# Performance work log

Hardware: AMD Instinct MI355X
Metric: run time of the kernel (lower is better)

## Reference

```python
import jax, jax.numpy as jnp
import numpy as np

B, S, D, H, R, N, RK = 2, 2048, 1024, 16, 64, 32, 128
DH = D // H
EPS = 1e-5


def setup_inputs() -> dict:
    key = jax.random.key(0)
    ks = jax.random.split(key, 24)
    f = lambda i, shape, sc=1.0: jax.random.normal(ks[i], shape, dtype=jnp.float32) * sc
    sm = lambda i, shape: jax.nn.softmax(f(i, shape), axis=-1)
    return {
        'x': f(0, (B, S, D)),
        'f_qk': f(1, (N, D, R), 0.02), 'f_v': f(2, (N, D, R), 0.02),
        'r_qk': f(3, (N, R, D), 0.02), 'r_v': f(4, (N, R, D), 0.02),
        'f_know': f(5, (N, D, RK), 0.02), 'r_know': f(6, (N, RK, D), 0.02),
        'W_O': f(7, (D, D), 0.02),
        'gamma1': jnp.ones(D, jnp.float32), 'beta1': jnp.zeros(D, jnp.float32),
        'gamma2': jnp.ones(D, jnp.float32), 'beta2': jnp.zeros(D, jnp.float32),
        'w_fq': sm(8, (B, S, N)), 'w_fk': sm(9, (B, S, N)), 'w_fv': sm(10, (B, S, N)),
        'w_rq': sm(11, (B, S, N)), 'w_rk': sm(12, (B, S, N)), 'w_rv': sm(13, (B, S, N)),
        'w_know_f': sm(14, (B, S, N)), 'w_know_r': sm(15, (B, S, N)),
    }


def _ln(x, g, b):
    mu = jnp.mean(x, axis=-1, keepdims=True)
    var = jnp.mean(jnp.square(x - mu), axis=-1, keepdims=True)
    return g * (x - mu) * jax.lax.rsqrt(var + EPS) + b


def _feature(x, neurons, w):
    # x [B,S,D], neurons [N,D,R], w [B,S,N] -> [B,S,R]
    all_h = jnp.einsum('bsd,ndr->bsnr', x, neurons)
    return jnp.einsum('bsnr,bsn->bsr', all_h, w)


def _restore(h, neurons, w):
    # h [B,S,R], neurons [N,R,D], w [B,S,N] -> [B,S,D]
    # fuse: avoid materializing [B,S,N,D]; outer-product [B,S,N,R] is small
    t = w[..., None] * h[:, :, None, :]
    return jnp.einsum('bsnr,nrd->bsd', t, neurons)


def _causal_attn(Q, K, V):
    # Q,K,V: [B,H,S,DH]
    scale = 1.0 / jnp.sqrt(jnp.asarray(DH, Q.dtype))
    scores = jnp.einsum('bhqd,bhkd->bhqk', Q, K) * scale
    mask = jnp.tril(jnp.ones((S, S), bool))
    scores = jnp.where(mask, scores, jnp.asarray(-jnp.inf, scores.dtype))
    probs = jax.nn.softmax(scores, axis=-1)
    return jnp.einsum('bhqk,bhkd->bhqd', probs, V)


def reference(x, f_qk, f_v, r_qk, r_v, f_know, r_know, W_O,
              gamma1, beta1, gamma2, beta2,
              w_fq, w_fk, w_fv, w_rq, w_rk, w_rv, w_know_f, w_know_r):
    # --- attention circuit ---
    nx = _ln(x, gamma1, beta1)
    h_q = _feature(nx, f_qk, w_fq)
    h_k = _feature(nx, f_qk, w_fk)
    h_v = _feature(nx, f_v, w_fv)
    Q = _restore(h_q, r_qk, w_rq)
    K = _restore(h_k, r_qk, w_rk)
    V = _restore(h_v, r_v, w_rv)
    to_heads = lambda t: t.reshape(B, S, H, DH).transpose(0, 2, 1, 3)
    attn = _causal_attn(to_heads(Q), to_heads(K), to_heads(V))
    attn = attn.transpose(0, 2, 1, 3).reshape(B, S, D)
    attn_out = attn @ W_O.T  # nn.Linear(d_model, d_model, bias=False)
    x = x + attn_out
    # --- knowledge circuit ---
    nx2 = _ln(x, gamma2, beta2)
    h = _feature(nx2, f_know, w_know_f)
    know_out = _restore(h, r_know, w_know_r)
    x = x + know_out
    return x
```

## Files before the change

### kernel.cpp

```cpp
#include <hip/hip_runtime.h>
#include <stdint.h>


typedef __bf16 bf16x8 __attribute__((ext_vector_type(8)));
typedef float f32x4 __attribute__((ext_vector_type(4)));

__device__ __forceinline__ unsigned short f2b(float f) {
  union { float f; unsigned u; } v; v.f = f;
  unsigned u = v.u;
  unsigned r = (u + 0x7FFFu + ((u >> 16) & 1u)) >> 16;
  return (unsigned short)r;
}
__device__ __forceinline__ float b2f(unsigned short h) {
  union { unsigned u; float f; } v; v.u = ((unsigned)h) << 16;
  return v.f;
}
__device__ __forceinline__ unsigned pk2(float lo, float hi) {
  return (unsigned)f2b(lo) | ((unsigned)f2b(hi) << 16);
}
__device__ __forceinline__ unsigned pkt(float lo, float hi) {
  union { float f; unsigned u; } a, b; a.f = lo; b.f = hi;
  return __builtin_amdgcn_perm(b.u, a.u, 0x07060302u);
}

__global__ __launch_bounds__(256, 3) void gemm_bt(
    const unsigned short* __restrict__ A, const unsigned short* __restrict__ Bt,
    void* __restrict__ out, int M, int N, int K) {
  __shared__ unsigned short lsA[128 * 64];
  __shared__ unsigned short lsB[128 * 64];
  const int tid = threadIdx.x;
  const int w = tid >> 6, lane = tid & 63;
  const int quad = lane >> 4, l16 = lane & 15;
  const int wr = w >> 1, wc = w & 1;
  const int row0 = blockIdx.y * 128;
  const int col0 = blockIdx.x * 128;

  const int srow = w * 32 + (lane >> 3);
  const int scg = ((lane & 7) ^ (lane >> 3)) * 8;
  const unsigned short* ap = A + (size_t)(row0 + srow) * K + scg;
  const unsigned short* bp = Bt + (size_t)(col0 + srow) * K + scg;

  const f32x4 fz = {0.f, 0.f, 0.f, 0.f};
  f32x4 acc[4][4];
#pragma unroll
  for (int i = 0; i < 4; ++i)
#pragma unroll
    for (int j = 0; j < 4; ++j) acc[i][j] = fz;

  for (int k0 = 0; k0 < K; k0 += 64) {
#pragma unroll
    for (int i = 0; i < 4; ++i) {
      __builtin_amdgcn_global_load_lds(
          (const __attribute__((address_space(1))) unsigned int*)(ap + (size_t)i * 8 * K + k0),
          (__attribute__((address_space(3))) unsigned int*)&lsA[(w * 32 + i * 8) * 64],
          16, 0, 0);
      __builtin_amdgcn_global_load_lds(
          (const __attribute__((address_space(1))) unsigned int*)(bp + (size_t)i * 8 * K + k0),
          (__attribute__((address_space(3))) unsigned int*)&lsB[(w * 32 + i * 8) * 64],
          16, 0, 0);
    }
    __syncthreads();
#pragma unroll
    for (int kk = 0; kk < 2; ++kk) {
      bf16x8 af[4], bfr[4];
      const int sl = (((kk * 4 + quad) ^ (l16 & 7)) * 8);
#pragma unroll
      for (int mt = 0; mt < 4; ++mt)
        af[mt] = *(const bf16x8*)&lsA[(wr * 64 + mt * 16 + l16) * 64 + sl];
#pragma unroll
      for (int nt = 0; nt < 4; ++nt)
        bfr[nt] = *(const bf16x8*)&lsB[(wc * 64 + nt * 16 + l16) * 64 + sl];
#pragma unroll
      for (int mt = 0; mt < 4; ++mt)
#pragma unroll
        for (int nt = 0; nt < 4; ++nt)
          acc[mt][nt] = __builtin_amdgcn_mfma_f32_16x16x32_bf16(af[mt], bfr[nt], acc[mt][nt], 0, 0, 0);
    }
    __syncthreads();
  }

  const int rb = row0 + wr * 64;
  const int cb = col0 + wc * 64;
#pragma unroll
  for (int mt = 0; mt < 4; ++mt) {
#pragma unroll
    for (int nt = 0; nt < 4; ++nt) {
      const int r = rb + mt * 16 + quad * 4;
      const int c = cb + nt * 16 + l16;
#pragma unroll
      for (int i = 0; i < 4; ++i)
        ((unsigned short*)out)[(size_t)(r + i) * N + c] = f2b(acc[mt][nt][i]);
    }
  }
}

__global__ __launch_bounds__(256, 3) void gemm_qkv(
    const unsigned short* __restrict__ t_qk, const unsigned short* __restrict__ t_v,
    const unsigned short* __restrict__ r_qkT, const unsigned short* __restrict__ r_vT,
    unsigned short* __restrict__ QK, unsigned short* __restrict__ VT) {
  __shared__ unsigned short lsA[128 * 64];
  __shared__ unsigned short lsB[128 * 64];
  const int K = 2048;
  const int bid = blockIdx.x;
  const unsigned short* A;
  const unsigned short* Bt;
  int row0, col0, isv;
  if (bid < 256) {
    const int xcd = bid & 7, j = bid >> 3;
    row0 = (xcd * 4 + (j >> 3)) * 128;
    col0 = (j & 7) * 128;
    A = t_v; Bt = r_vT; isv = 1;
  } else {
    const int u = bid - 256;
    const int xcd = u & 7, j = u >> 3;
    row0 = (xcd * 8 + (j >> 3)) * 128;
    col0 = (j & 7) * 128;
    A = t_qk; Bt = r_qkT; isv = 0;
  }
  const int tid = threadIdx.x;
  const int w = tid >> 6, lane = tid & 63;
  const int quad = lane >> 4, l16 = lane & 15;
  const int wr = w >> 1, wc = w & 1;

  const int srow = w * 32 + (lane >> 3);
  const int scg = ((lane & 7) ^ (lane >> 3)) * 8;
  const unsigned short* ap = A + (size_t)(row0 + srow) * K + scg;
  const unsigned short* bp = Bt + (size_t)(col0 + srow) * K + scg;

  const f32x4 fz = {0.f, 0.f, 0.f, 0.f};
  f32x4 acc[4][4];
#pragma unroll
  for (int i = 0; i < 4; ++i)
#pragma unroll
    for (int jj = 0; jj < 4; ++jj) acc[i][jj] = fz;

  for (int k0 = 0; k0 < K; k0 += 64) {
#pragma unroll
    for (int i = 0; i < 4; ++i) {
      __builtin_amdgcn_global_load_lds(
          (const __attribute__((address_space(1))) unsigned int*)(ap + (size_t)i * 8 * K + k0),
          (__attribute__((address_space(3))) unsigned int*)&lsA[(w * 32 + i * 8) * 64],
          16, 0, 0);
      __builtin_amdgcn_global_load_lds(
          (const __attribute__((address_space(1))) unsigned int*)(bp + (size_t)i * 8 * K + k0),
          (__attribute__((address_space(3))) unsigned int*)&lsB[(w * 32 + i * 8) * 64],
          16, 0, 0);
    }
    __syncthreads();
#pragma unroll
    for (int kk = 0; kk < 2; ++kk) {
      bf16x8 af[4], bfr[4];
      const int sl = (((kk * 4 + quad) ^ (l16 & 7)) * 8);
#pragma unroll
      for (int mt = 0; mt < 4; ++mt)
        af[mt] = *(const bf16x8*)&lsA[(wr * 64 + mt * 16 + l16) * 64 + sl];
#pragma unroll
      for (int nt = 0; nt < 4; ++nt)
        bfr[nt] = *(const bf16x8*)&lsB[(wc * 64 + nt * 16 + l16) * 64 + sl];
#pragma unroll
      for (int mt = 0; mt < 4; ++mt)
#pragma unroll
        for (int nt = 0; nt < 4; ++nt)
          acc[mt][nt] = __builtin_amdgcn_mfma_f32_16x16x32_bf16(af[mt], bfr[nt], acc[mt][nt], 0, 0, 0);
    }
    __syncthreads();
  }

  const int rb = row0 + wr * 64;
  const int cb = col0 + wc * 64;
#pragma unroll
  for (int mt = 0; mt < 4; ++mt) {
#pragma unroll
    for (int nt = 0; nt < 4; ++nt) {
      const int r = rb + mt * 16 + quad * 4;
      const int c = cb + nt * 16 + l16;
#pragma unroll
      for (int i = 0; i < 4; ++i) {
        const float v = acc[mt][nt][i];
        if (isv) VT[(size_t)c * 4096 + (r + i)] = f2b(v);
        else QK[(size_t)(r + i) * 1024 + c] = f2b(v);
      }
    }
  }
}

__global__ __launch_bounds__(256, 3) void gemm_ks4(
    const unsigned short* __restrict__ A, const unsigned short* __restrict__ Bt,
    float* __restrict__ p0, float* __restrict__ p1,
    float* __restrict__ p2, float* __restrict__ p3, int K) {
  __shared__ unsigned short lsA[128 * 64];
  __shared__ unsigned short lsB[128 * 64];
  const int N = 1024;
  const int bid = blockIdx.x;
  const int xcd = bid & 7, j = bid >> 3;
  const int row_l = j >> 5, rem = j & 31;
  const int ks = rem >> 3, col = rem & 7;
  const int row0 = (xcd * 4 + row_l) * 128;
  const int col0 = col * 128;
  const int kq = K >> 2;
  const int kbeg = ks * kq, kend = kbeg + kq;
  const int tid = threadIdx.x;
  const int w = tid >> 6, lane = tid & 63;
  const int quad = lane >> 4, l16 = lane & 15;
  const int wr = w >> 1, wc = w & 1;

  const int srow = w * 32 + (lane >> 3);
  const int scg = ((lane & 7) ^ (lane >> 3)) * 8;
  const unsigned short* ap = A + (size_t)(row0 + srow) * K + scg;
  const unsigned short* bp = Bt + (size_t)(col0 + srow) * K + scg;

  const f32x4 fz = {0.f, 0.f, 0.f, 0.f};
  f32x4 acc[4][4];
#pragma unroll
  for (int i = 0; i < 4; ++i)
#pragma unroll
    for (int jj = 0; jj < 4; ++jj) acc[i][jj] = fz;

  for (int k0 = kbeg; k0 < kend; k0 += 64) {
#pragma unroll
    for (int i = 0; i < 4; ++i) {
      __builtin_amdgcn_global_load_lds(
          (const __attribute__((address_space(1))) unsigned int*)(ap + (size_t)i * 8 * K + k0),
          (__attribute__((address_space(3))) unsigned int*)&lsA[(w * 32 + i * 8) * 64],
          16, 0, 0);
      __builtin_amdgcn_global_load_lds(
          (const __attribute__((address_space(1))) unsigned int*)(bp + (size_t)i * 8 * K + k0),
          (__attribute__((address_space(3))) unsigned int*)&lsB[(w * 32 + i * 8) * 64],
          16, 0, 0);
    }
    __syncthreads();
#pragma unroll
    for (int kk = 0; kk < 2; ++kk) {
      bf16x8 af[4], bfr[4];
      const int sl = (((kk * 4 + quad) ^ (l16 & 7)) * 8);
#pragma unroll
      for (int mt = 0; mt < 4; ++mt)
        af[mt] = *(const bf16x8*)&lsA[(wr * 64 + mt * 16 + l16) * 64 + sl];
#pragma unroll
      for (int nt = 0; nt < 4; ++nt)
        bfr[nt] = *(const bf16x8*)&lsB[(wc * 64 + nt * 16 + l16) * 64 + sl];
#pragma unroll
      for (int mt = 0; mt < 4; ++mt)
#pragma unroll
        for (int nt = 0; nt < 4; ++nt)
          acc[mt][nt] = __builtin_amdgcn_mfma_f32_16x16x32_bf16(af[mt], bfr[nt], acc[mt][nt], 0, 0, 0);
    }
    __syncthreads();
  }

  float* out = (ks == 0) ? p0 : (ks == 1) ? p1 : (ks == 2) ? p2 : p3;
  const int rb = row0 + wr * 64;
  const int cb = col0 + wc * 64;
#pragma unroll
  for (int mt = 0; mt < 4; ++mt) {
#pragma unroll
    for (int nt = 0; nt < 4; ++nt) {
      const int r = rb + mt * 16 + quad * 4;
      const int c = cb + nt * 16 + l16;
#pragma unroll
      for (int i = 0; i < 4; ++i)
        out[(size_t)(r + i) * N + c] = acc[mt][nt][i];
    }
  }
}

__global__ __launch_bounds__(256) void gemm_wo_res(
    const unsigned short* __restrict__ A, const unsigned short* __restrict__ Bt,
    const float* __restrict__ res, float* __restrict__ out) {
  __shared__ unsigned short lsA[128 * 64];
  __shared__ unsigned short lsB[64 * 64];
  const int K = 1024, N = 1024;
  const int bid = blockIdx.x;
  const int xcd = bid & 7, j = bid >> 3;
  const int row0 = (xcd * 4 + (j & 3)) * 128;
  const int col0 = (j >> 2) * 64;
  const int tid = threadIdx.x;
  const int w = tid >> 6, lane = tid & 63;
  const int quad = lane >> 4, l16 = lane & 15;
  const int wr = w >> 1, wc = w & 1;

  const int srowA = w * 32 + (lane >> 3);
  const int srowB = w * 16 + (lane >> 3);
  const int scg = ((lane & 7) ^ (lane >> 3)) * 8;
  const unsigned short* ap = A + (size_t)(row0 + srowA) * K + scg;
  const unsigned short* bp = Bt + (size_t)(col0 + srowB) * K + scg;

  const f32x4 fz = {0.f, 0.f, 0.f, 0.f};
  f32x4 acc[4][2];
#pragma unroll
  for (int i = 0; i < 4; ++i)
#pragma unroll
    for (int jj = 0; jj < 2; ++jj) acc[i][jj] = fz;

  for (int k0 = 0; k0 < K; k0 += 64) {
#pragma unroll
    for (int i = 0; i < 4; ++i)
      __builtin_amdgcn_global_load_lds(
          (const __attribute__((address_space(1))) unsigned int*)(ap + (size_t)i * 8 * K + k0),
          (__attribute__((address_space(3))) unsigned int*)&lsA[(w * 32 + i * 8) * 64],
          16, 0, 0);
#pragma unroll
    for (int i = 0; i < 2; ++i)
      __builtin_amdgcn_global_load_lds(
          (const __attribute__((address_space(1))) unsigned int*)(bp + (size_t)i * 8 * K + k0),
          (__attribute__((address_space(3))) unsigned int*)&lsB[(w * 16 + i * 8) * 64],
          16, 0, 0);
    __syncthreads();
#pragma unroll
    for (int kk = 0; kk < 2; ++kk) {
      bf16x8 af[4], bfr[2];
      const int sl = (((kk * 4 + quad) ^ (l16 & 7)) * 8);
#pragma unroll
      for (int mt = 0; mt < 4; ++mt)
        af[mt] = *(const bf16x8*)&lsA[(wr * 64 + mt * 16 + l16) * 64 + sl];
#pragma unroll
      for (int nt = 0; nt < 2; ++nt)
        bfr[nt] = *(const bf16x8*)&lsB[(wc * 32 + nt * 16 + l16) * 64 + sl];
#pragma unroll
      for (int mt = 0; mt < 4; ++mt)
#pragma unroll
        for (int nt = 0; nt < 2; ++nt)
          acc[mt][nt] = __builtin_amdgcn_mfma_f32_16x16x32_bf16(af[mt], bfr[nt], acc[mt][nt], 0, 0, 0);
    }
    __syncthreads();
  }

  const int rb = row0 + wr * 64;
  const int cb = col0 + wc * 32;
#pragma unroll
  for (int mt = 0; mt < 4; ++mt) {
#pragma unroll
    for (int nt = 0; nt < 2; ++nt) {
      const int r = rb + mt * 16 + quad * 4;
      const int c = cb + nt * 16 + l16;
#pragma unroll
      for (int i = 0; i < 4; ++i)
        out[(size_t)(r + i) * N + c] = acc[mt][nt][i] + res[(size_t)(r + i) * N + c];
    }
  }
}

__global__ __launch_bounds__(256) void reduce_add5(
    const float* __restrict__ p0, const float* __restrict__ p1,
    const float* __restrict__ p2, const float* __restrict__ p3,
    const float* __restrict__ res, float* __restrict__ out) {
  const int i = (blockIdx.x * 256 + threadIdx.x) * 4;
  const f32x4 a = *(const f32x4*)&p0[i];
  const f32x4 b = *(const f32x4*)&p1[i];
  const f32x4 c = *(const f32x4*)&p2[i];
  const f32x4 d = *(const f32x4*)&p3[i];
  const f32x4 e = *(const f32x4*)&res[i];
  f32x4 o;
#pragma unroll
  for (int k = 0; k < 4; ++k) o[k] = ((a[k] + b[k]) + (c[k] + d[k])) + e[k];
  *(f32x4*)&out[i] = o;
}

__global__ __launch_bounds__(256) void ln_kernel(
    const float* __restrict__ x, const float* __restrict__ g,
    const float* __restrict__ be, unsigned short* __restrict__ out) {
  __shared__ float sbuf[4];
  const int t = blockIdx.x, tid = threadIdx.x;
  const float* row = x + (size_t)t * 1024;
  float v[4], s = 0.f;
#pragma unroll
  for (int j = 0; j < 4; ++j) { v[j] = row[tid + j * 256]; s += v[j]; }
#pragma unroll
  for (int off = 32; off; off >>= 1) s += __shfl_xor(s, off);
  if ((tid & 63) == 0) sbuf[tid >> 6] = s;
  __syncthreads();
  const float mu = (sbuf[0] + sbuf[1] + sbuf[2] + sbuf[3]) * (1.f / 1024.f);
  __syncthreads();
  float ss = 0.f;
#pragma unroll
  for (int j = 0; j < 4; ++j) { const float d = v[j] - mu; ss += d * d; }
#pragma unroll
  for (int off = 32; off; off >>= 1) ss += __shfl_xor(ss, off);
  if ((tid & 63) == 0) sbuf[tid >> 6] = ss;
  __syncthreads();
  const float var = (sbuf[0] + sbuf[1] + sbuf[2] + sbuf[3]) * (1.f / 1024.f);
  const float rstd = rsqrtf(var + 1e-5f);
  unsigned short* orow = out + (size_t)t * 1024;
#pragma unroll
  for (int j = 0; j < 4; ++j) {
    const int c = tid + j * 256;
    orow[c] = f2b((v[j] - mu) * rstd * g[c] + be[c]);
  }
}

__global__ __launch_bounds__(256) void mix_attn(
    const unsigned short* __restrict__ all_h,
    const float* __restrict__ w_fq, const float* __restrict__ w_fk,
    const float* __restrict__ w_fv, const float* __restrict__ w_rq,
    const float* __restrict__ w_rk, const float* __restrict__ w_rv,
    unsigned short* __restrict__ t_qk, unsigned short* __restrict__ t_v) {
  __shared__ float hq[64], hk[64], hv[64];
  const int t = blockIdx.x, tid = threadIdx.x;
  const int wvi = tid >> 6, lane = tid & 63;
  const unsigned short* row = all_h + (size_t)t * 4096;
  if (wvi < 3) {
    const float* wf = (wvi == 0 ? w_fq : wvi == 1 ? w_fk : w_fv) + (size_t)t * 32;
    const int base = (wvi == 2) ? 2048 : 0;
    float acc = 0.f;
#pragma unroll
    for (int n = 0; n < 32; ++n) acc += wf[n] * b2f(row[base + n * 64 + lane]);
    (wvi == 0 ? hq : wvi == 1 ? hk : hv)[lane] = acc;
  }
  __syncthreads();
  const int n = tid >> 3, r0 = (tid & 7) * 8;
  const float wq = w_rq[(size_t)t * 32 + n];
  const float wk = w_rk[(size_t)t * 32 + n];
  const float wv2 = w_rv[(size_t)t * 32 + n];
  unsigned dq[4], dk[4], dv[4];
#pragma unroll
  for (int jj = 0; jj < 4; ++jj) {
    dq[jj] = pk2(wq * hq[r0 + 2 * jj], wq * hq[r0 + 2 * jj + 1]);
    dk[jj] = pk2(wk * hk[r0 + 2 * jj], wk * hk[r0 + 2 * jj + 1]);
    dv[jj] = pk2(wv2 * hv[r0 + 2 * jj], wv2 * hv[r0 + 2 * jj + 1]);
  }
  *(uint4*)&t_qk[(size_t)t * 2048 + tid * 8] = *(uint4*)dq;
  *(uint4*)&t_qk[(size_t)(4096 + t) * 2048 + tid * 8] = *(uint4*)dk;
  *(uint4*)&t_v[(size_t)t * 2048 + tid * 8] = *(uint4*)dv;
}

__global__ __launch_bounds__(256) void mix_know(
    const unsigned short* __restrict__ all_h, const float* __restrict__ w_f,
    const float* __restrict__ w_r, unsigned short* __restrict__ t_know) {
  __shared__ float h[128];
  const int t = blockIdx.x, tid = threadIdx.x;
  const unsigned short* row = all_h + (size_t)t * 4096;
  if (tid < 128) {
    const float* wf = w_f + (size_t)t * 32;
    float acc = 0.f;
#pragma unroll
    for (int n = 0; n < 32; ++n) acc += wf[n] * b2f(row[n * 128 + tid]);
    h[tid] = acc;
  }
  __syncthreads();
  const int n = tid >> 3, r0 = (tid & 7) * 16;
  const float wn = w_r[(size_t)t * 32 + n];
  unsigned d[8];
#pragma unroll
  for (int jj = 0; jj < 8; ++jj)
    d[jj] = pk2(wn * h[r0 + 2 * jj], wn * h[r0 + 2 * jj + 1]);
  *(uint4*)&t_know[(size_t)t * 4096 + tid * 16] = *(uint4*)d;
  *(uint4*)&t_know[(size_t)t * 4096 + tid * 16 + 8] = *(uint4*)&d[4];
}

__global__ __launch_bounds__(256) void prep_all(
    const float* __restrict__ f_qk, const float* __restrict__ f_v,
    const float* __restrict__ f_know, const float* __restrict__ r_qk,
    const float* __restrict__ r_v, const float* __restrict__ r_know,
    const float* __restrict__ W_O,
    unsigned short* __restrict__ fcomb, unsigned short* __restrict__ fknowT,
    unsigned short* __restrict__ r_qkT, unsigned short* __restrict__ r_vT,
    unsigned short* __restrict__ r_knowT, unsigned short* __restrict__ WO_bf) {
  __shared__ float tile[32][33];
  const int bid = blockIdx.x;
  const int tx = threadIdx.x, ty = threadIdx.y;
  const float* in;
  unsigned short* out;
  int R, C, gx, loc;
  if (bid < 2048)       { in = f_qk;   out = fcomb;                         R = 1024; C = 64;   gx = 2;  loc = bid; }
  else if (bid < 4096)  { in = f_v;    out = fcomb + (size_t)2048 * 1024;   R = 1024; C = 64;   gx = 2;  loc = bid - 2048; }
  else if (bid < 8192)  { in = f_know; out = fknowT;                        R = 1024; C = 128;  gx = 4;  loc = bid - 4096; }
  else if (bid < 10240) { in = r_qk;   out = r_qkT;                         R = 2048; C = 1024; gx = 32; loc = bid - 8192; }
  else if (bid < 12288) { in = r_v;    out = r_vT;                          R = 2048; C = 1024; gx = 32; loc = bid - 10240; }
  else if (bid < 16384) { in = r_know; out = r_knowT;                       R = 4096; C = 1024; gx = 32; loc = bid - 12288; }
  else {
    const int i = ((bid - 16384) * 256 + ty * 32 + tx) * 4;
    const f32x4 v = *(const f32x4*)&W_O[i];
    *(unsigned*)&WO_bf[i] = pk2(v[0], v[1]);
    *(unsigned*)&WO_bf[i + 2] = pk2(v[2], v[3]);
    return;
  }
  const int tiles = gx * (R >> 5);
  const int bb = loc / tiles, rem = loc % tiles;
  const int r0 = (rem / gx) * 32, c0 = (rem % gx) * 32;
  const float* ip = in + (size_t)bb * R * C;
  unsigned short* op = out + (size_t)bb * R * C;
#pragma unroll
  for (int j = 0; j < 4; ++j)
    tile[ty + j * 8][tx] = ip[(size_t)(r0 + ty + j * 8) * C + c0 + tx];
  __syncthreads();
#pragma unroll
  for (int j = 0; j < 4; ++j)
    op[(size_t)(c0 + ty + j * 8) * R + r0 + tx] = f2b(tile[tx][ty + j * 8]);
}

__global__ __launch_bounds__(256) void flash_split(
    const unsigned short* __restrict__ Q, const unsigned short* __restrict__ Kp,
    const unsigned short* __restrict__ VT, unsigned short* __restrict__ O,
    float* __restrict__ Opart, float* __restrict__ ml) {
  __shared__ unsigned short Kls[2][64 * 64];
  __shared__ unsigned short Vls[2][64 * 64];
  const int uidx = 79 - (int)blockIdx.x;
  int uu = uidx, qt = 0, ch = 0;
  for (int q = 0; q < 32; ++q) {
    const int n = (q >> 3) + 1;
    if (uu < n) { qt = q; ch = uu; break; }
    uu -= n;
  }
  const int bh = blockIdx.y;
  const int b = bh >> 4, h = bh & 15;
  const int tid = threadIdx.x;
  const int w = tid >> 6, lane = tid & 63, quad = lane >> 4, l16 = lane & 15;
  const int tb = b * 2048;
  const int qrow = qt * 64 + w * 16;
  const int ktlo = ch * 8;
  const int kthi = min(qt, ch * 8 + 7);
  const float C = 0.18033688f;

  const int srow = (lane >> 3);
  const int scol = ((lane & 7) ^ srow) * 8;

  bf16x8 qf[2];
#pragma unroll
  for (int kk = 0; kk < 2; ++kk)
    qf[kk] = *(const bf16x8*)&Q[(size_t)(tb + qrow + l16) * 1024 + h * 64 + kk * 32 + quad * 8];

  const f32x4 fz = {0.f, 0.f, 0.f, 0.f};
  float m_i = -1e30f, l_i = 0.f;
  f32x4 o_acc[4];
#pragma unroll
  for (int nt = 0; nt < 4; ++nt) o_acc[nt] = fz;

  auto stage = [&](int buf, int kt) {
#pragma unroll
    for (int j = 0; j < 2; ++j) {
      const int rg = (w * 2 + j) * 8 + srow;
      __builtin_amdgcn_global_load_lds(
          (const __attribute__((address_space(1))) unsigned int*)
              (Kp + (size_t)(tb + kt * 64 + rg) * 1024 + h * 64 + scol),
          (__attribute__((address_space(3))) unsigned int*)&Kls[buf][(w * 2 + j) * 8 * 64],
          16, 0, 0);
      __builtin_amdgcn_global_load_lds(
          (const __attribute__((address_space(1))) unsigned int*)
              (VT + (size_t)(h * 64 + rg) * 4096 + tb + kt * 64 + scol),
          (__attribute__((address_space(3))) unsigned int*)&Vls[buf][(w * 2 + j) * 8 * 64],
          16, 0, 0);
    }
  };

  const int srcA = (((quad & 1) * 32 + l16) << 2);
  const int srcB = srcA + 64;
  const bool hiq = (quad >= 2);

  stage(0, ktlo);
  __syncthreads();
  int buf = 0;
  for (int kt = ktlo; kt <= kthi; ++kt) {
    bf16x8 kf[8], vf[8];
#pragma unroll
    for (int kk = 0; kk < 2; ++kk)
#pragma unroll
      for (int nt = 0; nt < 4; ++nt) {
        const int sl = (((kk * 4 + quad) ^ (l16 & 7)) * 8);
        kf[kk * 4 + nt] = *(const bf16x8*)&Kls[buf][(nt * 16 + l16) * 64 + sl];
        vf[kk * 4 + nt] = *(const bf16x8*)&Vls[buf][(nt * 16 + l16) * 64 + sl];
      }
    if (kt < kthi) stage(buf ^ 1, kt + 1);

    const bool diag = (kt == qt);
    const int ntmax = diag ? (w + 1) : 4;
    f32x4 s[4];
#pragma unroll
    for (int nt = 0; nt < 4; ++nt) s[nt] = fz;
    __builtin_amdgcn_s_setprio(1);
#pragma unroll
    for (int kk = 0; kk < 2; ++kk)
#pragma unroll
      for (int nt = 0; nt < 4; ++nt)
        if (nt < ntmax)
          s[nt] = __builtin_amdgcn_mfma_f32_16x16x32_bf16(kf[kk * 4 + nt], qf[kk], s[nt], 0, 0, 0);
    __builtin_amdgcn_s_setprio(0);

    const int qloc = w * 16 + l16;
    float mxs[4] = {-1e30f, -1e30f, -1e30f, -1e30f};
#pragma unroll
    for (int nt = 0; nt < 4; ++nt) {
      if (nt >= ntmax) continue;
#pragma unroll
      for (int i = 0; i < 4; ++i) {
        float v = s[nt][i];
        if (diag && (nt * 16 + quad * 4 + i) > qloc) v = -1e30f;
        s[nt][i] = v;
        mxs[nt] = fmaxf(mxs[nt], v);
      }
    }
    float mx = fmaxf(fmaxf(mxs[0], mxs[1]), fmaxf(mxs[2], mxs[3]));
    mx = fmaxf(mx, __shfl_xor(mx, 16));
    mx = fmaxf(mx, __shfl_xor(mx, 32));
    if (!__all(mx <= m_i)) {
      const float mn = fmaxf(m_i, mx);
      const float al = exp2f((m_i - mn) * C);
      m_i = mn;
      l_i *= al;
#pragma unroll
      for (int nt = 0; nt < 4; ++nt)
#pragma unroll
        for (int i = 0; i < 4; ++i) o_acc[nt][i] *= al;
    }
    const float mC = m_i * C;
    float rsv[4] = {0.f, 0.f, 0.f, 0.f};
#pragma unroll
    for (int nt = 0; nt < 4; ++nt) {
      if (nt >= ntmax) {
#pragma unroll
        for (int i = 0; i < 4; ++i) s[nt][i] = 0.f;
        continue;
      }
#pragma unroll
      for (int i = 0; i < 4; ++i) {
        const float p = exp2f(fmaf(s[nt][i], C, -mC));
        s[nt][i] = p;
        rsv[nt] += p;
      }
    }
    float rs = (rsv[0] + rsv[1]) + (rsv[2] + rsv[3]);
    rs += __shfl_xor(rs, 16);
    rs += __shfl_xor(rs, 32);
    l_i += rs;

    unsigned pk[4][2];
#pragma unroll
    for (int nt = 0; nt < 4; ++nt) {
      pk[nt][0] = pkt(s[nt][0], s[nt][1]);
      pk[nt][1] = pkt(s[nt][2], s[nt][3]);
    }
#pragma unroll
    for (int kk = 0; kk < 2; ++kk) {
      const int ea = 2 * kk, eb = 2 * kk + 1;
      const unsigned u0 = __builtin_amdgcn_ds_bpermute(srcA, pk[ea][0]);
      const unsigned u1 = __builtin_amdgcn_ds_bpermute(srcA, pk[ea][1]);
      const unsigned u2 = __builtin_amdgcn_ds_bpermute(srcB, pk[ea][0]);
      const unsigned u3 = __builtin_amdgcn_ds_bpermute(srcB, pk[ea][1]);
      const unsigned w0 = __builtin_amdgcn_ds_bpermute(srcA, pk[eb][0]);
      const unsigned w1 = __builtin_amdgcn_ds_bpermute(srcA, pk[eb][1]);
      const unsigned w2 = __builtin_amdgcn_ds_bpermute(srcB, pk[eb][0]);
      const unsigned w3 = __builtin_amdgcn_ds_bpermute(srcB, pk[eb][1]);
      unsigned dw[4];
      dw[0] = hiq ? w0 : u0;
      dw[1] = hiq ? w1 : u1;
      dw[2] = hiq ? w2 : u2;
      dw[3] = hiq ? w3 : u3;
      const bf16x8 pf = *(const bf16x8*)dw;
      __builtin_amdgcn_s_setprio(1);
#pragma unroll
      for (int nt = 0; nt < 4; ++nt)
        o_acc[nt] = __builtin_amdgcn_mfma_f32_16x16x32_bf16(vf[kk * 4 + nt], pf, o_acc[nt], 0, 0, 0);
      __builtin_amdgcn_s_setprio(0);
    }
    __syncthreads();
    buf ^= 1;
  }

  const int nch = (qt >> 3) + 1;
  if (nch == 1) {
    const float inv = 1.0f / l_i;
    unsigned short* orow = O + (size_t)(tb + qrow + l16) * 1024 + h * 64;
#pragma unroll
    for (int nt = 0; nt < 4; ++nt) {
      const unsigned d0 = pk2(o_acc[nt][0] * inv, o_acc[nt][1] * inv);
      const unsigned d1 = pk2(o_acc[nt][2] * inv, o_acc[nt][3] * inv);
      *(unsigned*)&orow[nt * 16 + quad * 4] = d0;
      *(unsigned*)&orow[nt * 16 + quad * 4 + 2] = d1;
    }
  } else {
    const int slot = bh * 80 + uidx;
    const int lq = w * 16 + l16;
    float* op = Opart + ((size_t)slot * 64 + lq) * 64;
#pragma unroll
    for (int nt = 0; nt < 4; ++nt)
      *(f32x4*)&op[nt * 16 + quad * 4] = o_acc[nt];
    if (quad == 0) {
      ml[(size_t)slot * 128 + lq * 2] = m_i;
      ml[(size_t)slot * 128 + lq * 2 + 1] = l_i;
    }
  }
}

__global__ __launch_bounds__(256) void flash_reduce(
    const float* __restrict__ Opart, const float* __restrict__ ml,
    unsigned short* __restrict__ O) {
  const int qt = 8 + blockIdx.x;
  const int bh = blockIdx.y;
  const int b = bh >> 4, h = bh & 15;
  const int j = qt >> 3;
  const int base = 8 * (j * (j + 1) / 2) + (qt - 8 * j) * (j + 1);
  const int nch = j + 1;
  const int tid = threadIdx.x;
  const int lq = tid >> 2, dq = (tid & 3) * 16;
  const float C = 0.18033688f;

  float mc[4], lc[4];
  float m = -1e30f;
#pragma unroll
  for (int c = 0; c < 4; ++c) {
    if (c < nch) {
      const size_t sl = (size_t)(bh * 80 + base + c) * 128 + lq * 2;
      mc[c] = ml[sl];
      lc[c] = ml[sl + 1];
    } else { mc[c] = -1e30f; lc[c] = 0.f; }
    m = fmaxf(m, mc[c]);
  }
  float fac[4], lt = 0.f;
#pragma unroll
  for (int c = 0; c < 4; ++c) {
    fac[c] = (c < nch) ? exp2f((mc[c] - m) * C) : 0.f;
    lt += fac[c] * lc[c];
  }
  const float inv = 1.0f / lt;
  float acc[16];
#pragma unroll
  for (int i = 0; i < 16; ++i) acc[i] = 0.f;
#pragma unroll
  for (int c = 0; c < 4; ++c) {
    if (c >= nch) continue;
    const float* op = Opart + ((size_t)(bh * 80 + base + c) * 64 + lq) * 64 + dq;
#pragma unroll
    for (int i = 0; i < 16; i += 4) {
      const f32x4 v = *(const f32x4*)&op[i];
#pragma unroll
      for (int k = 0; k < 4; ++k) acc[i + k] += fac[c] * v[k];
    }
  }
  unsigned short* orow = O + (size_t)(b * 2048 + qt * 64 + lq) * 1024 + h * 64 + dq;
#pragma unroll
  for (int i = 0; i < 16; i += 2)
    *(unsigned*)&orow[i] = pk2(acc[i] * inv, acc[i + 1] * inv);
}

extern "C" void kernel_launch(void* const* d_in, const int* in_sizes, int n_in,
                              void* d_out, int out_size, void* d_ws, size_t ws_size,
                              hipStream_t stream) {
  (void)in_sizes; (void)n_in; (void)out_size; (void)ws_size;
  const float* x      = (const float*)d_in[0];
  const float* f_qk   = (const float*)d_in[1];
  const float* f_v    = (const float*)d_in[2];
  const float* r_qk   = (const float*)d_in[3];
  const float* r_v    = (const float*)d_in[4];
  const float* f_know = (const float*)d_in[5];
  const float* r_know = (const float*)d_in[6];
  const float* W_O    = (const float*)d_in[7];
  const float* gamma1 = (const float*)d_in[8];
  const float* beta1  = (const float*)d_in[9];
  const float* gamma2 = (const float*)d_in[10];
  const float* beta2  = (const float*)d_in[11];
  const float* w_fq   = (const float*)d_in[12];
  const float* w_fk   = (const float*)d_in[13];
  const float* w_fv   = (const float*)d_in[14];
  const float* w_rq   = (const float*)d_in[15];
  const float* w_rk   = (const float*)d_in[16];
  const float* w_rv   = (const float*)d_in[17];
  const float* w_kf   = (const float*)d_in[18];
  const float* w_kr   = (const float*)d_in[19];

  char* base = (char*)d_ws;
  size_t off = 0;
  auto alloc = [&](size_t b) { char* p = base + off; off += (b + 255) & ~(size_t)255; return p; };
  unsigned short* fcomb   = (unsigned short*)alloc(8388608);
  unsigned short* fknowT  = (unsigned short*)alloc(8388608);
  unsigned short* r_qkT   = (unsigned short*)alloc(4194304);
  unsigned short* r_vT    = (unsigned short*)alloc(4194304);
  unsigned short* r_knowT = (unsigned short*)alloc(8388608);
  unsigned short* WO_bf   = (unsigned short*)alloc(2097152);
  unsigned short* nx_bf   = (unsigned short*)alloc(8388608);
  unsigned short* all_h   = (unsigned short*)alloc(33554432);
  unsigned short* t_qk    = (unsigned short*)alloc(33554432);
  unsigned short* t_v     = (unsigned short*)alloc(16777216);
  unsigned short* QKbuf   = (unsigned short*)alloc(16777216);
  unsigned short* VT      = (unsigned short*)alloc(8388608);
  unsigned short* attn    = (unsigned short*)alloc(8388608);
  float* x1 = (float*)t_v;
  float* Opart = (float*)all_h;
  float* mlbuf = (float*)((char*)all_h + 41943040);
  float* pW0 = (float*)all_h;
  float* pW1 = (float*)((char*)all_h + 16777216);
  float* pW2 = (float*)QKbuf;
  float* pW3_know = (float*)VT;

  const dim3 blk256(256), blkT(32, 8);

  prep_all<<<17408, blkT, 0, stream>>>(f_qk, f_v, f_know, r_qk, r_v, r_know, W_O,
                                       fcomb, fknowT, r_qkT, r_vT, r_knowT, WO_bf);

  ln_kernel<<<4096, blk256, 0, stream>>>(x, gamma1, beta1, nx_bf);
  gemm_bt<<<dim3(32, 32), blk256, 0, stream>>>(nx_bf, fcomb, all_h, 4096, 4096, 1024);
  mix_attn<<<4096, blk256, 0, stream>>>(all_h, w_fq, w_fk, w_fv, w_rq, w_rk, w_rv, t_qk, t_v);
  gemm_qkv<<<768, blk256, 0, stream>>>(t_qk, t_v, r_qkT, r_vT, QKbuf, VT);
  flash_split<<<dim3(80, 32), blk256, 0, stream>>>(QKbuf, QKbuf + (size_t)4096 * 1024, VT, attn,
                                                   Opart, mlbuf);
  flash_reduce<<<dim3(24, 32), blk256, 0, stream>>>(Opart, mlbuf, attn);
  gemm_wo_res<<<512, blk256, 0, stream>>>(attn, WO_bf, x, x1);

  ln_kernel<<<4096, blk256, 0, stream>>>(x1, gamma2, beta2, nx_bf);
  gemm_bt<<<dim3(32, 32), blk256, 0, stream>>>(nx_bf, fknowT, all_h, 4096, 4096, 1024);
  mix_know<<<4096, blk256, 0, stream>>>(all_h, w_kf, w_kr, t_qk);
  gemm_ks4<<<1024, blk256, 0, stream>>>(t_qk, r_knowT, pW0, pW1, pW2, pW3_know, 4096);
  reduce_add5<<<4096, blk256, 0, stream>>>(pW0, pW1, pW2, pW3_know, x1, (float*)d_out);
}
```

Baseline: 495.9 us.

## Remap GEMM blocks per XCD and peel diagonal tile out of flash loop

The big gemm_bt launches become a 1D grid whose block index is remapped so that each XCD handles four contiguous row-tiles, meant to improve L2 reuse of the A rows within each die's cache. In flash_split, the causal diagonal key tile is peeled out of the main loop, so off-diagonal iterations run without masking or ntmax checks and use vectorised max and exp code. The next-tile prefetch is also issued before the LDS fragment reads. The remap hardcodes N=4096 and a 32x32 tile grid, and the peeled diagonal path duplicates code.

```diff
diff --git a/kernel.cpp b/kernel.cpp
--- a/kernel.cpp
+++ b/kernel.cpp
@@ -22,18 +22,27 @@
   union { float f; unsigned u; } a, b; a.f = lo; b.f = hi;
   return __builtin_amdgcn_perm(b.u, a.u, 0x07060302u);
 }
+__device__ __forceinline__ f32x4 vmax4(f32x4 a, f32x4 b) {
+  f32x4 r;
+  r[0] = fmaxf(a[0], b[0]); r[1] = fmaxf(a[1], b[1]);
+  r[2] = fmaxf(a[2], b[2]); r[3] = fmaxf(a[3], b[3]);
+  return r;
+}
 
 __global__ __launch_bounds__(256, 3) void gemm_bt(
     const unsigned short* __restrict__ A, const unsigned short* __restrict__ Bt,
-    void* __restrict__ out, int M, int N, int K) {
+    void* __restrict__ out, int K) {
   __shared__ unsigned short lsA[128 * 64];
   __shared__ unsigned short lsB[128 * 64];
+  const int N = 4096;
+  const int bid = blockIdx.x;
+  const int xcd = bid & 7, j = bid >> 3;
+  const int row0 = (xcd * 4 + (j >> 5)) * 128;
+  const int col0 = (j & 31) * 128;
   const int tid = threadIdx.x;
   const int w = tid >> 6, lane = tid & 63;
   const int quad = lane >> 4, l16 = lane & 15;
   const int wr = w >> 1, wc = w & 1;
-  const int row0 = blockIdx.y * 128;
-  const int col0 = blockIdx.x * 128;
 
   const int srow = w * 32 + (lane >> 3);
   const int scg = ((lane & 7) ^ (lane >> 3)) * 8;
@@ -45,7 +54,7 @@
 #pragma unroll
   for (int i = 0; i < 4; ++i)
 #pragma unroll
-    for (int j = 0; j < 4; ++j) acc[i][j] = fz;
+    for (int jj = 0; jj < 4; ++jj) acc[i][jj] = fz;
 
   for (int k0 = 0; k0 < K; k0 += 64) {
 #pragma unroll
@@ -546,82 +555,7 @@
   const int srcB = srcA + 64;
   const bool hiq = (quad >= 2);
 
-  stage(0, ktlo);
-  __syncthreads();
-  int buf = 0;
-  for (int kt = ktlo; kt <= kthi; ++kt) {
-    bf16x8 kf[8], vf[8];
-#pragma unroll
-    for (int kk = 0; kk < 2; ++kk)
-#pragma unroll
-      for (int nt = 0; nt < 4; ++nt) {
-        const int sl = (((kk * 4 + quad) ^ (l16 & 7)) * 8);
-        kf[kk * 4 + nt] = *(const bf16x8*)&Kls[buf][(nt * 16 + l16) * 64 + sl];
-        vf[kk * 4 + nt] = *(const bf16x8*)&Vls[buf][(nt * 16 + l16) * 64 + sl];
-      }
-    if (kt < kthi) stage(buf ^ 1, kt + 1);
-
-    const bool diag = (kt == qt);
-    const int ntmax = diag ? (w + 1) : 4;
-    f32x4 s[4];
-#pragma unroll
-    for (int nt = 0; nt < 4; ++nt) s[nt] = fz;
-    __builtin_amdgcn_s_setprio(1);
-#pragma unroll
-    for (int kk = 0; kk < 2; ++kk)
-#pragma unroll
-      for (int nt = 0; nt < 4; ++nt)
-        if (nt < ntmax)
-          s[nt] = __builtin_amdgcn_mfma_f32_16x16x32_bf16(kf[kk * 4 + nt], qf[kk], s[nt], 0, 0, 0);
-    __builtin_amdgcn_s_setprio(0);
-
-    const int qloc = w * 16 + l16;
-    float mxs[4] = {-1e30f, -1e30f, -1e30f, -1e30f};
-#pragma unroll
-    for (int nt = 0; nt < 4; ++nt) {
-      if (nt >= ntmax) continue;
-#pragma unroll
-      for (int i = 0; i < 4; ++i) {
-        float v = s[nt][i];
-        if (diag && (nt * 16 + quad * 4 + i) > qloc) v = -1e30f;
-        s[nt][i] = v;
-        mxs[nt] = fmaxf(mxs[nt], v);
-      }
-    }
-    float mx = fmaxf(fmaxf(mxs[0], mxs[1]), fmaxf(mxs[2], mxs[3]));
-    mx = fmaxf(mx, __shfl_xor(mx, 16));
-    mx = fmaxf(mx, __shfl_xor(mx, 32));
-    if (!__all(mx <= m_i)) {
-      const float mn = fmaxf(m_i, mx);
-      const float al = exp2f((m_i - mn) * C);
-      m_i = mn;
-      l_i *= al;
-#pragma unroll
-      for (int nt = 0; nt < 4; ++nt)
-#pragma unroll
-        for (int i = 0; i < 4; ++i) o_acc[nt][i] *= al;
-    }
-    const float mC = m_i * C;
-    float rsv[4] = {0.f, 0.f, 0.f, 0.f};
-#pragma unroll
-    for (int nt = 0; nt < 4; ++nt) {
-      if (nt >= ntmax) {
-#pragma unroll
-        for (int i = 0; i < 4; ++i) s[nt][i] = 0.f;
-        continue;
-      }
-#pragma unroll
-      for (int i = 0; i < 4; ++i) {
-        const float p = exp2f(fmaf(s[nt][i], C, -mC));
-        s[nt][i] = p;
-        rsv[nt] += p;
-      }
-    }
-    float rs = (rsv[0] + rsv[1]) + (rsv[2] + rsv[3]);
-    rs += __shfl_xor(rs, 16);
-    rs += __shfl_xor(rs, 32);
-    l_i += rs;
-
+  auto pv_block = [&](f32x4* s, bf16x8* vf, const f32x4& rsv) {
     unsigned pk[4][2];
 #pragma unroll
     for (int nt = 0; nt < 4; ++nt) {
@@ -651,8 +585,129 @@
         o_acc[nt] = __builtin_amdgcn_mfma_f32_16x16x32_bf16(vf[kk * 4 + nt], pf, o_acc[nt], 0, 0, 0);
       __builtin_amdgcn_s_setprio(0);
     }
+    float rs = (rsv[0] + rsv[1]) + (rsv[2] + rsv[3]);
+    rs += __shfl_xor(rs, 16);
+    rs += __shfl_xor(rs, 32);
+    l_i += rs;
+  };
+
+  stage(0, ktlo);
+  __syncthreads();
+  int buf = 0;
+
+  const bool hasdiag = (ch == (qt >> 3));
+  const int ktnd = hasdiag ? kthi - 1 : kthi;
+
+  for (int kt = ktlo; kt <= ktnd; ++kt) {
+    if (kt < kthi) stage(buf ^ 1, kt + 1);
+    bf16x8 kf[8], vf[8];
+#pragma unroll
+    for (int kk = 0; kk < 2; ++kk)
+#pragma unroll
+      for (int nt = 0; nt < 4; ++nt) {
+        const int sl = (((kk * 4 + quad) ^ (l16 & 7)) * 8);
+        kf[kk * 4 + nt] = *(const bf16x8*)&Kls[buf][(nt * 16 + l16) * 64 + sl];
+        vf[kk * 4 + nt] = *(const bf16x8*)&Vls[buf][(nt * 16 + l16) * 64 + sl];
+      }
+
+    f32x4 s[4];
+    __builtin_amdgcn_s_setprio(1);
+#pragma unroll
+    for (int nt = 0; nt < 4; ++nt)
+      s[nt] = __builtin_amdgcn_mfma_f32_16x16x32_bf16(kf[nt], qf[0], fz, 0, 0, 0);
+#pragma unroll
+    for (int nt = 0; nt < 4; ++nt)
+      s[nt] = __builtin_amdgcn_mfma_f32_16x16x32_bf16(kf[4 + nt], qf[1], s[nt], 0, 0, 0);
+    __builtin_amdgcn_s_setprio(0);
+
+    const f32x4 m4 = vmax4(vmax4(s[0], s[1]), vmax4(s[2], s[3]));
+    float mx = fmaxf(fmaxf(m4[0], m4[1]), fmaxf(m4[2], m4[3]));
+    mx = fmaxf(mx, __shfl_xor(mx, 16));
+    mx = fmaxf(mx, __shfl_xor(mx, 32));
+    if (!__all(mx <= m_i)) {
+      const float mn = fmaxf(m_i, mx);
+      const float al = exp2f((m_i - mn) * C);
+      m_i = mn;
+      l_i *= al;
+#pragma unroll
+      for (int nt = 0; nt < 4; ++nt) o_acc[nt] *= al;
+    }
+    const float mC = m_i * C;
+    f32x4 rsv = fz;
+#pragma unroll
+    for (int nt = 0; nt < 4; ++nt) {
+      f32x4 e = s[nt] * C - mC;
+      f32x4 p;
+#pragma unroll
+      for (int i = 0; i < 4; ++i) p[i] = exp2f(e[i]);
+      s[nt] = p;
+      rsv += p;
+    }
+    pv_block(s, vf, rsv);
     __syncthreads();
     buf ^= 1;
+  }
+
+  if (hasdiag) {
+    bf16x8 kf[8], vf[8];
+#pragma unroll
+    for (int kk = 0; kk < 2; ++kk)
+#pragma unroll
+      for (int nt = 0; nt < 4; ++nt) {
+        const int sl = (((kk * 4 + quad) ^ (l16 & 7)) * 8);
+        kf[kk * 4 + nt] = *(const bf16x8*)&Kls[buf][(nt * 16 + l16) * 64 + sl];
+        vf[kk * 4 + nt] = *(const bf16x8*)&Vls[buf][(nt * 16 + l16) * 64 + sl];
+      }
+    const int ntmax = w + 1;
+    f32x4 s[4];
+#pragma unroll
+    for (int nt = 0; nt < 4; ++nt) s[nt] = fz;
+    __builtin_amdgcn_s_setprio(1);
+#pragma unroll
+    for (int kk = 0; kk < 2; ++kk)
+#pragma unroll
+      for (int nt = 0; nt < 4; ++nt)
+        if (nt < ntmax)
+          s[nt] = __builtin_amdgcn_mfma_f32_16x16x32_bf16(kf[kk * 4 + nt], qf[kk], s[nt], 0, 0, 0);
+    __builtin_amdgcn_s_setprio(0);
+
+    const int qloc = w * 16 + l16;
+    float mxs[4] = {-1e30f, -1e30f, -1e30f, -1e30f};
+#pragma unroll
+    for (int nt = 0; nt < 4; ++nt) {
+      if (nt >= ntmax) continue;
+#pragma unroll
+      for (int i = 0; i < 4; ++i) {
+        float v = s[nt][i];
+        if ((nt * 16 + quad * 4 + i) > qloc) v = -1e30f;
+        s[nt][i] = v;
+        mxs[nt] = fmaxf(mxs[nt], v);
+      }
+    }
+    float mx = fmaxf(fmaxf(mxs[0], mxs[1]), fmaxf(mxs[2], mxs[3]));
+    mx = fmaxf(mx, __shfl_xor(mx, 16));
+    mx = fmaxf(mx, __shfl_xor(mx, 32));
+    if (!__all(mx <= m_i)) {
+      const float mn = fmaxf(m_i, mx);
+      const float al = exp2f((m_i - mn) * C);
+      m_i = mn;
+      l_i *= al;
+#pragma unroll
+      for (int nt = 0; nt < 4; ++nt) o_acc[nt] *= al;
+    }
+    const float mC = m_i * C;
+    f32x4 rsv = fz;
+#pragma unroll
+    for (int nt = 0; nt < 4; ++nt) {
+      if (nt >= ntmax) { s[nt] = fz; continue; }
+      f32x4 e = s[nt] * C - mC;
+      f32x4 p;
+#pragma unroll
+      for (int i = 0; i < 4; ++i) p[i] = exp2f(e[i]);
+      s[nt] = p;
+      rsv += p;
+    }
+    pv_block(s, vf, rsv);
   }
 
   const int nch = (qt >> 3) + 1;
@@ -786,7 +841,7 @@
                                        fcomb, fknowT, r_qkT, r_vT, r_knowT, WO_bf);
 
   ln_kernel<<<4096, blk256, 0, stream>>>(x, gamma1, beta1, nx_bf);
-  gemm_bt<<<dim3(32, 32), blk256, 0, stream>>>(nx_bf, fcomb, all_h, 4096, 4096, 1024);
+  gemm_bt<<<1024, blk256, 0, stream>>>(nx_bf, fcomb, all_h, 1024);
   mix_attn<<<4096, blk256, 0, stream>>>(all_h, w_fq, w_fk, w_fv, w_rq, w_rk, w_rv, t_qk, t_v);
   gemm_qkv<<<768, blk256, 0, stream>>>(t_qk, t_v, r_qkT, r_vT, QKbuf, VT);
   flash_split<<<dim3(80, 32), blk256, 0, stream>>>(QKbuf, QKbuf + (size_t)4096 * 1024, VT, attn,
@@ -795,7 +850,7 @@
   gemm_wo_res<<<512, blk256, 0, stream>>>(attn, WO_bf, x, x1);
 
   ln_kernel<<<4096, blk256, 0, stream>>>(x1, gamma2, beta2, nx_bf);
-  gemm_bt<<<dim3(32, 32), blk256, 0, stream>>>(nx_bf, fknowT, all_h, 4096, 4096, 1024);
+  gemm_bt<<<1024, blk256, 0, stream>>>(nx_bf, fknowT, all_h, 1024);
   mix_know<<<4096, blk256, 0, stream>>>(all_h, w_kf, w_kr, t_qk);
   gemm_ks4<<<1024, blk256, 0, stream>>>(t_qk, r_knowT, pW0, pW1, pW2, pW3_know, 4096);
   reduce_add5<<<4096, blk256, 0, stream>>>(pW0, pW1, pW2, pW3_know, x1, (float*)d_out);
```

Measured after the change: 493.4 us. No clear change (-0.5%).
